# Optimization experiments

Hardware: AMD Instinct MI355X
Metric: run time of the kernel (lower is better)

## Reference

```python
import jax, jax.numpy as jnp
import numpy as np

B, S, E, H = 2, 2048, 1024, 16
D = E // H  # head_dim = 64


def setup_inputs() -> dict:
    key = jax.random.key(0)
    ks = jax.random.split(key, 9)
    sc = 1.0 / np.sqrt(E)
    return {
        "x": jax.random.normal(ks[0], (B, S, E), dtype=jnp.float32),
        "Wq": jax.random.normal(ks[1], (E, E), dtype=jnp.float32) * sc,
        "bq": jnp.zeros((E,), dtype=jnp.float32),
        "Wk": jax.random.normal(ks[2], (E, E), dtype=jnp.float32) * sc,
        "bk": jnp.zeros((E,), dtype=jnp.float32),
        "Wv": jax.random.normal(ks[3], (E, E), dtype=jnp.float32) * sc,
        "bv": jnp.zeros((E,), dtype=jnp.float32),
        "Wo": jax.random.normal(ks[4], (E, E), dtype=jnp.float32) * sc,
        "bo": jnp.zeros((E,), dtype=jnp.float32),
    }


def reference(x, Wq, bq, Wk, bk, Wv, bv, Wo, bo):
    b, s, e = x.shape
    # projections: [B,S,E] -> [B,H,S,D]
    def heads(w, bias):
        return (x @ w + bias).reshape(b, s, H, D).transpose(0, 2, 1, 3)
    q, k, v = heads(Wq, bq), heads(Wk, bk), heads(Wv, bv)
    # scores [B,H,S,S]
    scores = jnp.einsum("bhqd,bhkd->bhqk", q, k) / jnp.sqrt(jnp.float32(D))
    causal = jnp.tril(jnp.ones((s, s), dtype=bool))
    scores = jnp.where(causal[None, None], scores, -jnp.inf)
    weights = jax.nn.softmax(scores, axis=-1)
    out = jnp.einsum("bhqk,bhkd->bhqd", weights, v)
    out = out.transpose(0, 2, 1, 3).reshape(b, s, e)
    return out @ Wo + bo
```

## Files before the change

### kernel.cpp

```cpp
#include <hip/hip_runtime.h>
#include <hip/hip_bf16.h>

#define B_SZ 2
#define S_LEN 2048
#define E_DIM 1024
#define NH 16
#define DH 64
#define M_ROWS (B_SZ * S_LEN)
#define QB 128
#define KVB 64

typedef __attribute__((ext_vector_type(8))) short short8;
typedef __attribute__((ext_vector_type(4))) float floatx4;

static __device__ __forceinline__ unsigned short f2bf(float f) {
    __hip_bfloat16 h = __float2bfloat16(f);
    return *reinterpret_cast<unsigned short*>(&h);
}
static __device__ __forceinline__ float bf2f(unsigned short u) {
    unsigned int v = ((unsigned int)u) << 16;
    return __builtin_bit_cast(float, v);
}

static __device__ __forceinline__ void gl2lds16(const void* g, void* l) {
    __builtin_amdgcn_global_load_lds((const __attribute__((address_space(1))) void*)g,
                                     (__attribute__((address_space(3))) void*)l, 16, 0, 0);
}

#define WAIT_VM0() asm volatile("s_waitcnt vmcnt(0)" ::: "memory")
#define WAIT_LGKM0() asm volatile("s_waitcnt lgkmcnt(0)" ::: "memory")

__global__ __launch_bounds__(256) void prep(const float* __restrict__ x,
                                            unsigned short* __restrict__ Xb,
                                            const float* __restrict__ W0,
                                            const float* __restrict__ W1,
                                            const float* __restrict__ W2,
                                            const float* __restrict__ W3,
                                            unsigned short* __restrict__ T0,
                                            unsigned short* __restrict__ T1,
                                            unsigned short* __restrict__ T2,
                                            unsigned short* __restrict__ T3) {
    __shared__ float tile[32][33];
    int bid = blockIdx.x;
    int t = threadIdx.x;
    if (bid < 4096) {
        int i = (bid * 256 + t) * 4;
        float4 v = *reinterpret_cast<const float4*>(x + i);
        ushort4 o;
        o.x = f2bf(v.x); o.y = f2bf(v.y); o.z = f2bf(v.z); o.w = f2bf(v.w);
        *reinterpret_cast<ushort4*>(Xb + i) = o;
        return;
    }
    int u = bid - 4096;
    int z = u >> 10, rest = u & 1023;
    int bx = (rest & 31) * 32, by = (rest >> 5) * 32;
    const float* W = (z == 0) ? W0 : (z == 1) ? W1 : (z == 2) ? W2 : W3;
    unsigned short* Wt = (z == 0) ? T0 : (z == 1) ? T1 : (z == 2) ? T2 : T3;
    int tx = t & 31, ty = t >> 5;
#pragma unroll
    for (int i = 0; i < 32; i += 8)
        tile[ty + i][tx] = W[(size_t)(by + ty + i) * E_DIM + bx + tx];
    __syncthreads();
#pragma unroll
    for (int i = 0; i < 32; i += 8)
        Wt[(size_t)(bx + ty + i) * E_DIM + by + tx] = f2bf(tile[tx][ty + i]);
}

#define QSCALE 0.18033688011112042f

__global__ __launch_bounds__(512, 2) void gemm_qkv8(const unsigned short* __restrict__ Wcat,
                                                    const unsigned short* __restrict__ Xb,
                                                    const float* __restrict__ bq,
                                                    const float* __restrict__ bk,
                                                    const float* __restrict__ bv,
                                                    unsigned short* __restrict__ Qg,
                                                    unsigned short* __restrict__ Kg,
                                                    unsigned short* __restrict__ Vtg) {
    __shared__ __align__(16) char lds[2][2][32768];

    int t = threadIdx.x;
    int b = blockIdx.x;
    int xcd = b & 7, ii = b >> 3;
    int it = (xcd & 3) * 3 + (ii >> 3);
    int jt = (xcd >> 2) * 8 + (ii & 7);
    int iBase = it << 8, jBase = jt << 8;

    int w = t >> 6, lane = t & 63;
    int lr = lane & 15, lh = lane >> 4;
    int wm = w >> 2, wn = w & 3;

    int srow = t >> 3;
    int scbx = ((t & 7) << 4) ^ ((srow & 7) << 4);

    const char* Ab = (const char*)Wcat;
    const char* Bb = (const char*)Xb;

    floatx4 acc[8][4];
#pragma unroll
    for (int i = 0; i < 8; i++)
#pragma unroll
        for (int j = 0; j < 4; j++) acc[i][j] = (floatx4){0.f, 0.f, 0.f, 0.f};

    auto stageA = [&](int buf, int kt) {
        int k0b = kt << 7;
#pragma unroll
        for (int c = 0; c < 4; c++)
            gl2lds16(Ab + (size_t)(iBase + c * 64 + srow) * 2048 + k0b + scbx,
                     &lds[buf][0][c * 8192 + t * 16]);
    };
    auto stageB = [&](int buf, int kt) {
        int k0b = kt << 7;
#pragma unroll
        for (int c = 0; c < 4; c++)
            gl2lds16(Bb + (size_t)(jBase + c * 64 + srow) * 2048 + k0b + scbx,
                     &lds[buf][1][c * 8192 + t * 16]);
    };

    short8 af[4][2], bf[4][2];
    auto rdA = [&](int buf, int qm) {
#pragma unroll
        for (int mi = 0; mi < 4; mi++)
#pragma unroll
            for (int ks = 0; ks < 2; ks++) {
                int row = wm * 128 + qm * 64 + mi * 16 + lr;
                af[mi][ks] = *reinterpret_cast<const short8*>(
                    &lds[buf][0][(row * 128 + ks * 64 + lh * 16) ^ ((row & 7) << 4)]);
            }
    };
    auto rdB = [&](int buf, int qn) {
#pragma unroll
        for (int ni = 0; ni < 2; ni++)
#pragma unroll
            for (int ks = 0; ks < 2; ks++) {
                int row = wn * 64 + qn * 32 + ni * 16 + lr;
                bf[qn * 2 + ni][ks] = *reinterpret_cast<const short8*>(
                    &lds[buf][1][(row * 128 + ks * 64 + lh * 16) ^ ((row & 7) << 4)]);
            }
    };
    auto mfma16 = [&](int qm, int qn) {
        __builtin_amdgcn_s_setprio(1);
#pragma unroll
        for (int mi = 0; mi < 4; mi++)
#pragma unroll
            for (int ni = 0; ni < 2; ni++)
#pragma unroll
                for (int ks = 0; ks < 2; ks++)
                    acc[qm * 4 + mi][qn * 2 + ni] = __builtin_amdgcn_mfma_f32_16x16x32_bf16(
                        af[mi][ks], bf[qn * 2 + ni][ks], acc[qm * 4 + mi][qn * 2 + ni], 0, 0, 0);
        __builtin_amdgcn_s_setprio(0);
    };

    const int NT = 16;
    stageA(0, 0);
    stageB(0, 0);
    WAIT_VM0();
    __builtin_amdgcn_s_barrier();

    for (int kt = 0; kt < NT; ++kt) {
        int cur = kt & 1, nxt = cur ^ 1;
        bool pf = (kt + 1 < NT);
        rdA(cur, 0);
        rdB(cur, 0);
        if (pf) stageA(nxt, kt + 1);
        __builtin_amdgcn_s_barrier();
        WAIT_LGKM0();
        __builtin_amdgcn_sched_barrier(0);
        mfma16(0, 0);
        __builtin_amdgcn_s_barrier();
        rdB(cur, 1);
        if (pf) stageB(nxt, kt + 1);
        __builtin_amdgcn_s_barrier();
        WAIT_LGKM0();
        __builtin_amdgcn_sched_barrier(0);
        mfma16(0, 1);
        __builtin_amdgcn_s_barrier();
        rdA(cur, 1);
        __builtin_amdgcn_s_barrier();
        WAIT_LGKM0();
        __builtin_amdgcn_sched_barrier(0);
        mfma16(1, 0);
        __builtin_amdgcn_s_barrier();
        if (pf) WAIT_VM0();
        __builtin_amdgcn_s_barrier();
        mfma16(1, 1);
        __builtin_amdgcn_s_barrier();
    }

    int wsel = iBase >> 10;
    const float* bias = (wsel == 0) ? bq : (wsel == 1) ? bk : bv;
    __syncthreads();

    if (wsel < 2) {
        unsigned short* O = wsel ? Kg : Qg;
        float scale = wsel ? 1.0f : QSCALE;
#pragma unroll
        for (int mi8 = 0; mi8 < 8; mi8++) {
            int i = iBase + wm * 128 + mi8 * 16 + lh * 4;
            int im = i & 1023;
            int h = im >> 6, d0 = im & 63;
            float4 bs = *reinterpret_cast<const float4*>(&bias[im]);
#pragma unroll
            for (int nf = 0; nf < 4; nf++) {
                int j = jBase + wn * 64 + nf * 16 + lr;
                int b_ = j >> 11, s = j & (S_LEN - 1);
                ushort4 pk;
                pk.x = f2bf((acc[mi8][nf][0] + bs.x) * scale);
                pk.y = f2bf((acc[mi8][nf][1] + bs.y) * scale);
                pk.z = f2bf((acc[mi8][nf][2] + bs.z) * scale);
                pk.w = f2bf((acc[mi8][nf][3] + bs.w) * scale);
                *reinterpret_cast<ushort4*>(
                    &O[((size_t)(b_ * NH + h) * S_LEN + s) * DH + d0]) = pk;
            }
        }
    } else {
        char* lw = &lds[0][0][0] + w * 16384;
#pragma unroll
        for (int mi8 = 0; mi8 < 8; mi8++) {
            int i = iBase + wm * 128 + mi8 * 16 + lh * 4;
            float4 bs = *reinterpret_cast<const float4*>(&bias[i & 1023]);
#pragma unroll
            for (int nf = 0; nf < 4; nf++) {
                int jl = nf * 16 + lr;
#pragma unroll
                for (int r = 0; r < 4; r++) {
                    int il = mi8 * 16 + lh * 4 + r;
                    float bb = (r == 0) ? bs.x : (r == 1) ? bs.y : (r == 2) ? bs.z : bs.w;
                    *reinterpret_cast<unsigned short*>(
                        lw + ((il * 128 + jl * 2) ^ ((il & 7) << 4))) =
                        f2bf(acc[mi8][nf][r] + bb);
                }
            }
        }
        __syncthreads();
#pragma unroll
        for (int rep = 0; rep < 16; rep++) {
            int idx = rep * 64 + lane;
            int il = idx >> 3, jb = idx & 7;
            short8 vv = *reinterpret_cast<const short8*>(
                lw + ((il * 128 + jb * 16) ^ ((il & 7) << 4)));
            int i = iBase + wm * 128 + il;
            int im = i & 1023;
            int h = im >> 6, d = im & 63;
            int j = jBase + wn * 64 + jb * 8;
            int b_ = j >> 11, s = j & (S_LEN - 1);
            *reinterpret_cast<short8*>(
                &Vtg[((size_t)(b_ * NH + h) * DH + d) * S_LEN + s]) = vv;
        }
    }
}

template <int NI>
static __device__ __forceinline__ void gemm_tile_mainloop(
    const unsigned short* __restrict__ A, const unsigned short* __restrict__ Bt,
    int mBase, int nBase, char* ldsA, char* ldsB, floatx4 (&acc)[4][NI]) {
    const int K = E_DIM;
    int t = threadIdx.x;
    int w = t >> 6, lane = t & 63;
    int lr = lane & 15, lh = lane >> 4;
    int wm = w >> 1, wn = w & 1;
    const char* Ab = (const char*)A;
    const char* Bb = (const char*)Bt;
    int srow = t >> 3;
    int scb = ((t & 7) << 4) ^ ((srow & 7) << 4);

#pragma unroll
    for (int mi = 0; mi < 4; mi++)
#pragma unroll
        for (int ni = 0; ni < NI; ni++) acc[mi][ni] = (floatx4){0.f, 0.f, 0.f, 0.f};

    for (int kt = 0; kt < K / 64; ++kt) {
        int k0 = kt * 64;
#pragma unroll
        for (int i = 0; i < 4; i++)
            gl2lds16(Ab + (size_t)(mBase + i * 32 + srow) * (K * 2) + k0 * 2 + scb,
                     ldsA + i * 4096 + t * 16);
#pragma unroll
        for (int i = 0; i < NI; i++)
            gl2lds16(Bb + (size_t)(nBase + i * 32 + srow) * (K * 2) + k0 * 2 + scb,
                     ldsB + i * 4096 + t * 16);
        __syncthreads();
#pragma unroll
        for (int ks = 0; ks < 2; ks++) {
            short8 af[4], bfr[NI];
#pragma unroll
            for (int mi = 0; mi < 4; mi++) {
                int row = wm * 64 + mi * 16 + lr;
                af[mi] = *reinterpret_cast<const short8*>(
                    ldsA + ((row * 128 + ks * 64 + lh * 16) ^ ((row & 7) << 4)));
            }
#pragma unroll
            for (int ni = 0; ni < NI; ni++) {
                int row = wn * (NI * 16) + ni * 16 + lr;
                bfr[ni] = *reinterpret_cast<const short8*>(
                    ldsB + ((row * 128 + ks * 64 + lh * 16) ^ ((row & 7) << 4)));
            }
#pragma unroll
            for (int mi = 0; mi < 4; mi++)
#pragma unroll
                for (int ni = 0; ni < NI; ni++)
                    acc[mi][ni] = __builtin_amdgcn_mfma_f32_16x16x32_bf16(af[mi], bfr[ni],
                                                                          acc[mi][ni], 0, 0, 0);
        }
        __syncthreads();
    }
}

__global__ __launch_bounds__(256) void gemm_o(const unsigned short* __restrict__ Og,
                                              const unsigned short* __restrict__ Wot,
                                              const float* __restrict__ bo,
                                              float* __restrict__ out) {
    __shared__ __align__(16) char ldsA[16384];
    __shared__ __align__(16) char ldsB[8192];
    int bid = blockIdx.y * 16 + blockIdx.x;
    int xcd = bid & 7, ii = bid >> 3;
    int xx = ii & 15;
    int yy = (xcd << 2) | (ii >> 4);
    int nBase = xx << 6;
    int mBase = yy << 7;

    floatx4 acc[4][2];
    gemm_tile_mainloop<2>(Og, Wot, mBase, nBase, ldsA, ldsB, acc);

    int w = threadIdx.x >> 6, lane = threadIdx.x & 63;
    int lr = lane & 15, lh = lane >> 4;
    int wm = w >> 1, wn = w & 1;
#pragma unroll
    for (int mi = 0; mi < 4; mi++)
#pragma unroll
        for (int ni = 0; ni < 2; ni++)
#pragma unroll
            for (int r = 0; r < 4; r++) {
                int m = mBase + wm * 64 + mi * 16 + lh * 4 + r;
                int n = nBase + wn * 32 + ni * 16 + lr;
                out[(size_t)m * E_DIM + n] = acc[mi][ni][r] + bo[n];
            }
}

__global__ __launch_bounds__(256) void attn_fwd(const unsigned short* __restrict__ Qg,
                                                const unsigned short* __restrict__ Kg,
                                                const unsigned short* __restrict__ Vtg,
                                                unsigned short* __restrict__ Og,
                                                unsigned short* __restrict__ Opart,
                                                float* __restrict__ lpart) {
    __shared__ __align__(16) char kt_lds[2][KVB * 128];
    __shared__ __align__(16) char vt_lds[2][KVB * 128];
    __shared__ __align__(16) unsigned short p_lds[4][32][72];

    int bid = blockIdx.y * 24 + blockIdx.x;
    int xcd = bid & 7, ii = bid >> 3;
    int idx = ii % 24;
    int bh = (xcd << 2) + ii / 24;

    int qb, kt_lo, kt_hi, chunk;
    bool split;
    if (idx < 16) {
        split = true;
        qb = 8 + (idx & 7);
        chunk = idx >> 3;
        if (chunk == 0) { kt_lo = 0; kt_hi = qb; }
        else            { kt_lo = qb + 1; kt_hi = 2 * qb + 1; }
    } else {
        split = false; chunk = 0;
        qb = 23 - idx;
        kt_lo = 0; kt_hi = 2 * qb + 1;
    }

    int w = threadIdx.x >> 6, lane = threadIdx.x & 63;
    int lr = lane & 15, lh = lane >> 4;
    int q0 = qb * QB + w * 32;

    const char* Kb = (const char*)(Kg + (size_t)bh * S_LEN * DH);
    const char* Vb = (const char*)(Vtg + (size_t)bh * DH * S_LEN);
    const unsigned short* Qb = Qg + (size_t)bh * S_LEN * DH;

    int wi0 = w * 2;
    int srow0 = wi0 * 8 + (lane >> 3);
    int scol = (lane & 7) << 4;

    auto stage = [&](int buf, int kt) {
        int kv0 = kt * KVB;
#pragma unroll
        for (int i = 0; i < 2; ++i) {
            int row = srow0 + i * 8;
            int colb = scol ^ ((row & 7) << 4);
            gl2lds16(Kb + (size_t)(kv0 + row) * 128 + colb,
                     kt_lds[buf] + (wi0 + i) * 1024);
            gl2lds16(Vb + (size_t)row * (S_LEN * 2) + (size_t)kv0 * 2 + colb,
                     vt_lds[buf] + (wi0 + i) * 1024);
        }
    };

    short8 aq[2][2];
#pragma unroll
    for (int m = 0; m < 2; m++)
#pragma unroll
        for (int ks = 0; ks < 2; ks++)
            aq[m][ks] = *reinterpret_cast<const short8*>(
                Qb + (size_t)(q0 + m * 16 + lr) * DH + ks * 32 + lh * 8);

    floatx4 oacc[2][4];
    float lsum[2][4];
#pragma unroll
    for (int m = 0; m < 2; m++) {
#pragma unroll
        for (int dt = 0; dt < 4; dt++) oacc[m][dt] = (floatx4){0.f, 0.f, 0.f, 0.f};
#pragma unroll
        for (int r = 0; r < 4; r++) lsum[m][r] = 0.f;
    }

    stage(0, kt_lo);
    __syncthreads();
    int buf = 0;

    for (int kt = kt_lo; kt <= kt_hi; ++kt) {
        if (kt < kt_hi) stage(buf ^ 1, kt + 1);
        int kv0 = kt * KVB;
        bool skip = (kv0 > q0 + 31);
        if (!skip) {
            const char* Kt = kt_lds[buf];
            const char* Vt = vt_lds[buf];
            floatx4 sacc[2][4];
#pragma unroll
            for (int m = 0; m < 2; m++)
#pragma unroll
                for (int nt = 0; nt < 4; nt++) sacc[m][nt] = (floatx4){0.f, 0.f, 0.f, 0.f};
#pragma unroll
            for (int ks = 0; ks < 2; ks++)
#pragma unroll
                for (int nt = 0; nt < 4; nt++) {
                    int row = nt * 16 + lr;
                    int addr = (row * 128 + ks * 64 + lh * 16) ^ ((row & 7) << 4);
                    short8 bk = *reinterpret_cast<const short8*>(Kt + addr);
#pragma unroll
                    for (int m = 0; m < 2; m++)
                        sacc[m][nt] = __builtin_amdgcn_mfma_f32_16x16x32_bf16(
                            aq[m][ks], bk, sacc[m][nt], 0, 0, 0);
                }
            if (kv0 + KVB - 1 > q0) {
#pragma unroll
                for (int m = 0; m < 2; m++)
#pragma unroll
                    for (int nt = 0; nt < 4; nt++)
#pragma unroll
                        for (int r = 0; r < 4; r++) {
                            int qrow = q0 + m * 16 + lh * 4 + r;
                            int kcol = kv0 + nt * 16 + lr;
                            if (kcol > qrow) sacc[m][nt][r] = -1e30f;
                        }
            }
#pragma unroll
            for (int m = 0; m < 2; m++) {
                float rs[4] = {0.f, 0.f, 0.f, 0.f};
#pragma unroll
                for (int nt = 0; nt < 4; nt++)
#pragma unroll
                    for (int r = 0; r < 4; r++) {
                        float p = __builtin_amdgcn_exp2f(sacc[m][nt][r]);
                        rs[r] += p;
                        p_lds[w][m * 16 + lh * 4 + r][nt * 16 + lr] = f2bf(p);
                    }
#pragma unroll
                for (int r = 0; r < 4; r++) lsum[m][r] += rs[r];
            }
            WAIT_LGKM0();
            short8 pa[2][2];
#pragma unroll
            for (int m = 0; m < 2; m++)
#pragma unroll
                for (int ks = 0; ks < 2; ks++)
                    pa[m][ks] = *reinterpret_cast<const short8*>(
                        &p_lds[w][m * 16 + lr][ks * 32 + lh * 8]);
#pragma unroll
            for (int ks = 0; ks < 2; ks++)
#pragma unroll
                for (int dt = 0; dt < 4; dt++) {
                    int row = dt * 16 + lr;
                    int addr = (row * 128 + ks * 64 + lh * 16) ^ ((row & 7) << 4);
                    short8 bv = *reinterpret_cast<const short8*>(Vt + addr);
#pragma unroll
                    for (int m = 0; m < 2; m++)
                        oacc[m][dt] = __builtin_amdgcn_mfma_f32_16x16x32_bf16(
                            pa[m][ks], bv, oacc[m][dt], 0, 0, 0);
                }
        }
        __syncthreads();
        buf ^= 1;
    }

#pragma unroll
    for (int m = 0; m < 2; m++)
#pragma unroll
        for (int msk = 1; msk < 16; msk <<= 1)
#pragma unroll
            for (int r = 0; r < 4; r++) lsum[m][r] += __shfl_xor(lsum[m][r], msk);

    if (split) {
        int pi = ((bh << 3) + (qb - 8)) * 2 + chunk;
        unsigned short* Op = Opart + (size_t)pi * (QB * DH);
        float* lp = lpart + (size_t)pi * QB;
#pragma unroll
        for (int m = 0; m < 2; m++) {
#pragma unroll
            for (int r = 0; r < 4; r++) {
                int row = w * 32 + m * 16 + lh * 4 + r;
#pragma unroll
                for (int dt = 0; dt < 4; dt++)
                    Op[row * DH + dt * 16 + lr] = f2bf(oacc[m][dt][r]);
                if (lr == r) lp[row] = lsum[m][r];
            }
        }
    } else {
        int b_ = bh >> 4, h_ = bh & 15;
#pragma unroll
        for (int m = 0; m < 2; m++)
#pragma unroll
            for (int r = 0; r < 4; r++) {
                float inv = 1.f / lsum[m][r];
                int srow = q0 + m * 16 + lh * 4 + r;
#pragma unroll
                for (int dt = 0; dt < 4; dt++)
                    Og[((size_t)b_ * S_LEN + srow) * E_DIM + h_ * 64 + dt * 16 + lr] =
                        f2bf(oacc[m][dt][r] * inv);
            }
    }
}

__global__ __launch_bounds__(256) void attn_reduce(const unsigned short* __restrict__ Opart,
                                                   const float* __restrict__ lpart,
                                                   unsigned short* __restrict__ Og) {
    int bh = blockIdx.x;
    int qt = blockIdx.y;
    int t = threadIdx.x;
    int cg = t & 7, r0 = t >> 3;
    int pi0 = ((bh << 3) + qt) * 2;
    const unsigned short* A = Opart + (size_t)pi0 * (QB * DH);
    const unsigned short* Bp = A + (QB * DH);
    const float* lA = lpart + (size_t)pi0 * QB;
    const float* lB = lA + QB;
    int b_ = bh >> 4, h_ = bh & 15;
    int qrow0 = (8 + qt) * QB;
#pragma unroll
    for (int rr = 0; rr < 4; rr++) {
        int row = r0 + rr * 32;
        float inv = 1.f / (lA[row] + lB[row]);
        short8 va = *reinterpret_cast<const short8*>(A + row * DH + cg * 8);
        short8 vb = *reinterpret_cast<const short8*>(Bp + row * DH + cg * 8);
        short8 o;
#pragma unroll
        for (int j = 0; j < 8; j++)
            o[j] = (short)f2bf((bf2f((unsigned short)va[j]) + bf2f((unsigned short)vb[j])) * inv);
        *reinterpret_cast<short8*>(Og + ((size_t)b_ * S_LEN + qrow0 + row) * E_DIM +
                                   h_ * 64 + cg * 8) = o;
    }
}

extern "C" void kernel_launch(void* const* d_in, const int* in_sizes, int n_in,
                              void* d_out, int out_size, void* d_ws, size_t ws_size,
                              hipStream_t stream) {
    const float* x  = (const float*)d_in[0];
    const float* Wq = (const float*)d_in[1];
    const float* bq = (const float*)d_in[2];
    const float* Wk = (const float*)d_in[3];
    const float* bk = (const float*)d_in[4];
    const float* Wv = (const float*)d_in[5];
    const float* bv = (const float*)d_in[6];
    const float* Wo = (const float*)d_in[7];
    const float* bo = (const float*)d_in[8];
    float* out = (float*)d_out;

    const size_t NX = (size_t)M_ROWS * E_DIM;
    const size_t NW = (size_t)E_DIM * E_DIM;
    unsigned short* ws  = (unsigned short*)d_ws;
    unsigned short* Xb  = ws;
    unsigned short* Wqt = Xb + NX;
    unsigned short* Wkt = Wqt + NW;
    unsigned short* Wvt = Wkt + NW;
    unsigned short* Wot = Wvt + NW;
    unsigned short* Qg  = Wot + NW;
    unsigned short* Kg  = Qg + NX;
    unsigned short* Vtg = Kg + NX;
    unsigned short* Og  = Vtg + NX;
    unsigned short* Opart = Og + NX;
    float* lpart = (float*)(Opart + (size_t)512 * QB * DH);

    prep<<<dim3(8192), 256, 0, stream>>>(x, Xb, Wq, Wk, Wv, Wo, Wqt, Wkt, Wvt, Wot);

    gemm_qkv8<<<dim3(192), 512, 0, stream>>>(Wqt, Xb, bq, bk, bv, Qg, Kg, Vtg);

    attn_fwd<<<dim3(24, B_SZ * NH), 256, 0, stream>>>(Qg, Kg, Vtg, Og, Opart, lpart);
    attn_reduce<<<dim3(B_SZ * NH, 8), 256, 0, stream>>>(Opart, lpart, Og);

    gemm_o<<<dim3(E_DIM / 64, M_ROWS / 128), 256, 0, stream>>>(Og, Wot, bo, out);
}
```

Baseline: 109.1 us.

## Split attention KV ranges into up to three chunks and read V directly from global

Attention work is redistributed: query blocks 6-11 are split into two KV chunks and 12-15 into three, giving 960 blocks of more even size, and the reduce kernel combines two or three partials. V tiles are no longer staged through LDS but loaded straight from global memory into registers, overlapped with the QK MFMAs, which halves LDS use and allows a launch bound of four blocks per CU. The partial buffers now reuse the X bf16 workspace region. The risks are uncoalesced or latency-exposed V global loads and extra reduce traffic.

```diff
diff --git a/kernel.cpp b/kernel.cpp
--- a/kernel.cpp
+++ b/kernel.cpp
@@ -336,41 +336,34 @@
             }
 }
 
-__global__ __launch_bounds__(256) void attn_fwd(const unsigned short* __restrict__ Qg,
-                                                const unsigned short* __restrict__ Kg,
-                                                const unsigned short* __restrict__ Vtg,
-                                                unsigned short* __restrict__ Og,
-                                                unsigned short* __restrict__ Opart,
-                                                float* __restrict__ lpart) {
+__global__ __launch_bounds__(256, 4) void attn_fwd(const unsigned short* __restrict__ Qg,
+                                                   const unsigned short* __restrict__ Kg,
+                                                   const unsigned short* __restrict__ Vtg,
+                                                   unsigned short* __restrict__ Og,
+                                                   unsigned short* __restrict__ Opart,
+                                                   float* __restrict__ lpart) {
     __shared__ __align__(16) char kt_lds[2][KVB * 128];
-    __shared__ __align__(16) char vt_lds[2][KVB * 128];
     __shared__ __align__(16) unsigned short p_lds[4][32][72];
 
-    int bid = blockIdx.y * 24 + blockIdx.x;
+    int bid = blockIdx.x;
     int xcd = bid & 7, ii = bid >> 3;
-    int idx = ii % 24;
-    int bh = (xcd << 2) + ii / 24;
-
-    int qb, kt_lo, kt_hi, chunk;
-    bool split;
-    if (idx < 16) {
-        split = true;
-        qb = 8 + (idx & 7);
-        chunk = idx >> 3;
-        if (chunk == 0) { kt_lo = 0; kt_hi = qb; }
-        else            { kt_lo = qb + 1; kt_hi = 2 * qb + 1; }
-    } else {
-        split = false; chunk = 0;
-        qb = 23 - idx;
-        kt_lo = 0; kt_hi = 2 * qb + 1;
-    }
+    int bh = (xcd << 2) + ii / 30;
+    int jj = 29 - (ii % 30);
+    int qb, ch, c;
+    if (jj < 6)        { qb = jj; ch = 0; c = 1; }
+    else if (jj < 18)  { int u = jj - 6;  qb = 6 + (u >> 1); ch = u & 1; c = 2; }
+    else               { int u = jj - 18; qb = 12 + u / 3;   ch = u % 3; c = 3; }
+    int T = 2 * qb + 2;
+    int kt_lo = ch * T / c;
+    int kt_hi = (ch + 1) * T / c - 1;
+    bool split = (c > 1);
 
     int w = threadIdx.x >> 6, lane = threadIdx.x & 63;
     int lr = lane & 15, lh = lane >> 4;
     int q0 = qb * QB + w * 32;
 
     const char* Kb = (const char*)(Kg + (size_t)bh * S_LEN * DH);
-    const char* Vb = (const char*)(Vtg + (size_t)bh * DH * S_LEN);
+    const unsigned short* Vbs = Vtg + (size_t)bh * DH * S_LEN;
     const unsigned short* Qb = Qg + (size_t)bh * S_LEN * DH;
 
     int wi0 = w * 2;
@@ -385,8 +378,6 @@
             int colb = scol ^ ((row & 7) << 4);
             gl2lds16(Kb + (size_t)(kv0 + row) * 128 + colb,
                      kt_lds[buf] + (wi0 + i) * 1024);
-            gl2lds16(Vb + (size_t)row * (S_LEN * 2) + (size_t)kv0 * 2 + colb,
-                     vt_lds[buf] + (wi0 + i) * 1024);
         }
     };
 
@@ -418,7 +409,11 @@
         bool skip = (kv0 > q0 + 31);
         if (!skip) {
             const char* Kt = kt_lds[buf];
-            const char* Vt = vt_lds[buf];
+            short8 vf0[4], vf1[4];
+#pragma unroll
+            for (int dt = 0; dt < 4; dt++)
+                vf0[dt] = *reinterpret_cast<const short8*>(
+                    Vbs + (size_t)(dt * 16 + lr) * S_LEN + kv0 + lh * 8);
             floatx4 sacc[2][4];
 #pragma unroll
             for (int m = 0; m < 2; m++)
@@ -436,6 +431,10 @@
                         sacc[m][nt] = __builtin_amdgcn_mfma_f32_16x16x32_bf16(
                             aq[m][ks], bk, sacc[m][nt], 0, 0, 0);
                 }
+#pragma unroll
+            for (int dt = 0; dt < 4; dt++)
+                vf1[dt] = *reinterpret_cast<const short8*>(
+                    Vbs + (size_t)(dt * 16 + lr) * S_LEN + kv0 + 32 + lh * 8);
             if (kv0 + KVB - 1 > q0) {
 #pragma unroll
                 for (int m = 0; m < 2; m++)
@@ -471,16 +470,13 @@
                     pa[m][ks] = *reinterpret_cast<const short8*>(
                         &p_lds[w][m * 16 + lr][ks * 32 + lh * 8]);
 #pragma unroll
-            for (int ks = 0; ks < 2; ks++)
-#pragma unroll
-                for (int dt = 0; dt < 4; dt++) {
-                    int row = dt * 16 + lr;
-                    int addr = (row * 128 + ks * 64 + lh * 16) ^ ((row & 7) << 4);
-                    short8 bv = *reinterpret_cast<const short8*>(Vt + addr);
-#pragma unroll
-                    for (int m = 0; m < 2; m++)
-                        oacc[m][dt] = __builtin_amdgcn_mfma_f32_16x16x32_bf16(
-                            pa[m][ks], bv, oacc[m][dt], 0, 0, 0);
+            for (int dt = 0; dt < 4; dt++)
+#pragma unroll
+                for (int m = 0; m < 2; m++) {
+                    oacc[m][dt] = __builtin_amdgcn_mfma_f32_16x16x32_bf16(
+                        pa[m][0], vf0[dt], oacc[m][dt], 0, 0, 0);
+                    oacc[m][dt] = __builtin_amdgcn_mfma_f32_16x16x32_bf16(
+                        pa[m][1], vf1[dt], oacc[m][dt], 0, 0, 0);
                 }
         }
         __syncthreads();
@@ -495,7 +491,8 @@
             for (int r = 0; r < 4; r++) lsum[m][r] += __shfl_xor(lsum[m][r], msk);
 
     if (split) {
-        int pi = ((bh << 3) + (qb - 8)) * 2 + chunk;
+        int base = (qb < 12) ? (qb - 6) * 2 : 12 + (qb - 12) * 3;
+        int pi = bh * 24 + base + ch;
         unsigned short* Op = Opart + (size_t)pi * (QB * DH);
         float* lp = lpart + (size_t)pi * QB;
 #pragma unroll
@@ -529,26 +526,36 @@
                                                    const float* __restrict__ lpart,
                                                    unsigned short* __restrict__ Og) {
     int bh = blockIdx.x;
-    int qt = blockIdx.y;
+    int qb = 6 + blockIdx.y;
+    int c = (qb < 12) ? 2 : 3;
+    int base = (qb < 12) ? (qb - 6) * 2 : 12 + (qb - 12) * 3;
+    int pi0 = bh * 24 + base;
+    const unsigned short* P0 = Opart + (size_t)pi0 * (QB * DH);
+    const float* l0 = lpart + (size_t)pi0 * QB;
     int t = threadIdx.x;
     int cg = t & 7, r0 = t >> 3;
-    int pi0 = ((bh << 3) + qt) * 2;
-    const unsigned short* A = Opart + (size_t)pi0 * (QB * DH);
-    const unsigned short* Bp = A + (QB * DH);
-    const float* lA = lpart + (size_t)pi0 * QB;
-    const float* lB = lA + QB;
     int b_ = bh >> 4, h_ = bh & 15;
-    int qrow0 = (8 + qt) * QB;
+    int qrow0 = qb * QB;
 #pragma unroll
     for (int rr = 0; rr < 4; rr++) {
         int row = r0 + rr * 32;
-        float inv = 1.f / (lA[row] + lB[row]);
-        short8 va = *reinterpret_cast<const short8*>(A + row * DH + cg * 8);
-        short8 vb = *reinterpret_cast<const short8*>(Bp + row * DH + cg * 8);
+        float ls = l0[row] + l0[QB + row];
+        if (c == 3) ls += l0[2 * QB + row];
+        float inv = 1.f / ls;
+        short8 v0 = *reinterpret_cast<const short8*>(P0 + row * DH + cg * 8);
+        short8 v1 = *reinterpret_cast<const short8*>(P0 + QB * DH + row * DH + cg * 8);
+        float s[8];
+#pragma unroll
+        for (int j = 0; j < 8; j++)
+            s[j] = bf2f((unsigned short)v0[j]) + bf2f((unsigned short)v1[j]);
+        if (c == 3) {
+            short8 v2 = *reinterpret_cast<const short8*>(P0 + 2 * QB * DH + row * DH + cg * 8);
+#pragma unroll
+            for (int j = 0; j < 8; j++) s[j] += bf2f((unsigned short)v2[j]);
+        }
         short8 o;
 #pragma unroll
-        for (int j = 0; j < 8; j++)
-            o[j] = (short)f2bf((bf2f((unsigned short)va[j]) + bf2f((unsigned short)vb[j])) * inv);
+        for (int j = 0; j < 8; j++) o[j] = (short)f2bf(s[j] * inv);
         *reinterpret_cast<short8*>(Og + ((size_t)b_ * S_LEN + qrow0 + row) * E_DIM +
                                    h_ * 64 + cg * 8) = o;
     }
@@ -580,15 +587,15 @@
     unsigned short* Kg  = Qg + NX;
     unsigned short* Vtg = Kg + NX;
     unsigned short* Og  = Vtg + NX;
-    unsigned short* Opart = Og + NX;
-    float* lpart = (float*)(Opart + (size_t)512 * QB * DH);
+    unsigned short* Opart = Xb;
+    float* lpart = (float*)(Opart + (size_t)32 * 24 * QB * DH);
 
     prep<<<dim3(8192), 256, 0, stream>>>(x, Xb, Wq, Wk, Wv, Wo, Wqt, Wkt, Wvt, Wot);
 
     gemm_qkv8<<<dim3(192), 512, 0, stream>>>(Wqt, Xb, bq, bk, bv, Qg, Kg, Vtg);
 
-    attn_fwd<<<dim3(24, B_SZ * NH), 256, 0, stream>>>(Qg, Kg, Vtg, Og, Opart, lpart);
-    attn_reduce<<<dim3(B_SZ * NH, 8), 256, 0, stream>>>(Opart, lpart, Og);
+    attn_fwd<<<dim3(960), 256, 0, stream>>>(Qg, Kg, Vtg, Og, Opart, lpart);
+    attn_reduce<<<dim3(B_SZ * NH, 10), 256, 0, stream>>>(Opart, lpart, Og);
 
     gemm_o<<<dim3(E_DIM / 64, M_ROWS / 128), 256, 0, stream>>>(Og, Wot, bo, out);
 }
```

Result: slower. 158.2 us (+45.0%).
